# Kernel tuning notes

Measured on AMD Instinct MI355X. Metric: run time of the kernel, lower is better.

Reference implementation:

```python
import jax, jax.numpy as jnp
import numpy as np

EMB = 1024
HEADS = 16
HEAD_SZ = EMB // HEADS
EPS = 1e-5


def _layernorm(x, g, b):
    mu = jnp.mean(x, axis=-1, keepdims=True)
    var = jnp.mean(jnp.square(x - mu), axis=-1, keepdims=True)
    return (x - mu) * jax.lax.rsqrt(var + EPS) * g + b


def setup_inputs() -> dict:
    key = jax.random.key(0)
    ks = jax.random.split(key, 12)
    s_in = 1.0 / np.sqrt(EMB)
    s_h = 1.0 / np.sqrt(4 * EMB)
    return {
        "x": jax.random.normal(ks[0], (4, 1024, EMB), jnp.float32),
        # per-head Q/K/V projections stacked: [H, EMB, HEAD_SZ], no bias
        "wq": jax.random.normal(ks[1], (HEADS, EMB, HEAD_SZ), jnp.float32) * s_in,
        "wk": jax.random.normal(ks[2], (HEADS, EMB, HEAD_SZ), jnp.float32) * s_in,
        "wv": jax.random.normal(ks[3], (HEADS, EMB, HEAD_SZ), jnp.float32) * s_in,
        "w_proj": jax.random.normal(ks[4], (EMB, EMB), jnp.float32) * s_in,
        "b_proj": jnp.zeros((EMB,), jnp.float32),
        "w1": jax.random.normal(ks[5], (EMB, 4 * EMB), jnp.float32) * s_in,
        "b1": jnp.zeros((4 * EMB,), jnp.float32),
        "w2": jax.random.normal(ks[6], (4 * EMB, EMB), jnp.float32) * s_h,
        "b2": jnp.zeros((EMB,), jnp.float32),
        "g1": jnp.ones((EMB,), jnp.float32),
        "be1": jnp.zeros((EMB,), jnp.float32),
        "g2": jnp.ones((EMB,), jnp.float32),
        "be2": jnp.zeros((EMB,), jnp.float32),
    }


def reference(x, wq, wk, wv, w_proj, b_proj, w1, b1, w2, b2, g1, be1, g2, be2):
    B, T, C = x.shape
    # --- self-attention (pre-norm) ---
    h = _layernorm(x, g1, be1)
    q = jnp.einsum("btc,hcd->bhtd", h, wq)
    k = jnp.einsum("btc,hcd->bhtd", h, wk)
    v = jnp.einsum("btc,hcd->bhtd", h, wv)
    scale = 1.0 / jnp.sqrt(jnp.asarray(HEAD_SZ, x.dtype))
    scores = jnp.einsum("bhtd,bhsd->bhts", q, k) * scale  # non-causal: SDPA called with no mask
    attn = jax.nn.softmax(scores, axis=-1)
    o = jnp.einsum("bhts,bhsd->bhtd", attn, v)
    o = o.transpose(0, 2, 1, 3).reshape(B, T, C)  # concat heads (same order as torch.cat)
    sa_out = o @ w_proj + b_proj
    x = x + sa_out
    # --- feed-forward; note ln2 applied twice, faithful to source ---
    t = _layernorm(x, g2, be2)
    t = _layernorm(t, g2, be2)
    ff = jax.nn.relu(t @ w1 + b1) @ w2 + b2
    return x + ff
```

## Files before the change

kernel.cpp:

```cpp
#include <hip/hip_runtime.h>
#include <hip/hip_bf16.h>
#include <math.h>
#include <stdint.h>

typedef __bf16 bf16_t;
typedef __bf16 bf16x4 __attribute__((ext_vector_type(4)));
typedef __bf16 bf16x8 __attribute__((ext_vector_type(8)));
typedef float floatx4 __attribute__((ext_vector_type(4)));

#define BM 128
#define BK 32

__device__ __forceinline__ size_t ftaddr(int m, int k, int KT) {
    return ((size_t)(m >> 4) * KT + (k >> 5)) * 512
         + (((k >> 3) & 3) * 16 + (m & 15)) * 8 + (k & 7);
}

__device__ __forceinline__ void gload16(const void* g, void* lds) {
    __builtin_amdgcn_global_load_lds(
        (__attribute__((address_space(1))) void*)(uintptr_t)g,
        (__attribute__((address_space(3))) void*)(uintptr_t)lds,
        16, 0, 0);
}

template<int N>
__device__ __forceinline__ void waitvm_barrier() {
    if constexpr (N == 0)       asm volatile("s_waitcnt vmcnt(0)\n\ts_barrier" ::: "memory");
    else if constexpr (N == 4)  asm volatile("s_waitcnt vmcnt(4)\n\ts_barrier" ::: "memory");
    else if constexpr (N == 6)  asm volatile("s_waitcnt vmcnt(6)\n\ts_barrier" ::: "memory");
    else if constexpr (N == 8)  asm volatile("s_waitcnt vmcnt(8)\n\ts_barrier" ::: "memory");
    else if constexpr (N == 12) asm volatile("s_waitcnt vmcnt(12)\n\ts_barrier" ::: "memory");
    else if constexpr (N == 16) asm volatile("s_waitcnt vmcnt(16)\n\ts_barrier" ::: "memory");
    else static_assert(N == 0, "unsupported vmcnt");
}

__device__ __forceinline__ void waitvm_barrier_rt(int n) {
    switch (n) {
    case 12: asm volatile("s_waitcnt vmcnt(12)\n\ts_barrier" ::: "memory"); break;
    case 8:  asm volatile("s_waitcnt vmcnt(8)\n\ts_barrier"  ::: "memory"); break;
    case 6:  asm volatile("s_waitcnt vmcnt(6)\n\ts_barrier"  ::: "memory"); break;
    case 4:  asm volatile("s_waitcnt vmcnt(4)\n\ts_barrier"  ::: "memory"); break;
    default: asm volatile("s_waitcnt vmcnt(0)\n\ts_barrier"  ::: "memory"); break;
    }
}

__global__ void prep_kernel(const float* __restrict__ wq, const float* __restrict__ wk,
                            const float* __restrict__ wv, const float* __restrict__ w_proj,
                            const float* __restrict__ w1, const float* __restrict__ w2,
                            bf16_t* __restrict__ WQKVT, bf16_t* __restrict__ WPROJT,
                            bf16_t* __restrict__ W1T, bf16_t* __restrict__ W2T,
                            const float* __restrict__ x, const float* __restrict__ g1,
                            const float* __restrict__ be1, bf16_t* __restrict__ HB)
{
    __shared__ __align__(16) char psm[33024];
    const int tid = threadIdx.x;
    if (blockIdx.x < 3072) {
        float (*tile)[65] = (float(*)[65])psm;
        const int idx = blockIdx.x;
        const float* in; bf16_t* out; int R, C, rt, ct; long nrow0;
        if (idx < 768) {
            const int z = idx >> 8;
            const int hd = (idx >> 4) & 15;
            rt = idx & 15; ct = 0; R = 1024; C = 64;
            in  = (z == 0 ? wq : z == 1 ? wk : wv) + hd * 65536;
            out = WQKVT; nrow0 = z * 1024 + hd * 64;
        } else if (idx < 1024) {
            const int t = idx - 768; rt = t & 15; ct = t >> 4; R = 1024; C = 1024;
            in = w_proj; out = WPROJT; nrow0 = 0;
        } else if (idx < 2048) {
            const int t = idx - 1024; rt = t & 15; ct = t >> 4; R = 1024; C = 4096;
            in = w1; out = W1T; nrow0 = 0;
        } else {
            const int t = idx - 2048; rt = t & 63; ct = t >> 6; R = 4096; C = 1024;
            in = w2; out = W2T; nrow0 = 0;
        }
        const int r0 = rt * 64, c0 = ct * 64;
        const int tr = tid >> 4;
        const int tc = (tid & 15) * 4;
#pragma unroll
        for (int rr = 0; rr < 4; rr++) {
            const int r = tr + rr * 16;
            const float4 v = *(const float4*)&in[(long)(r0 + r) * C + c0 + tc];
            tile[r][tc + 0] = v.x; tile[r][tc + 1] = v.y;
            tile[r][tc + 2] = v.z; tile[r][tc + 3] = v.w;
        }
        __syncthreads();
        const int KT = R >> 5;
        const int w = tid >> 6, l = tid & 63;
        const int c = l >> 4, rr2 = l & 15;
#pragma unroll
        for (int it = 0; it < 2; ++it) {
            const int t8 = it * 4 + w;
            const int kt = t8 >> 2;
            const int nb = t8 & 3;
            const long n = nrow0 + c0 + nb * 16 + rr2;
            const int k = r0 + kt * 32 + c * 8;
            bf16x8 o;
#pragma unroll
            for (int e = 0; e < 8; e++)
                o[e] = (bf16_t)tile[kt * 32 + c * 8 + e][nb * 16 + rr2];
            *(bf16x8*)&out[ftaddr((int)n, k, KT)] = o;
        }
    } else {
        bf16_t (*ybuf)[1032] = (bf16_t(*)[1032])psm;
        const int wave = tid >> 6, lane = tid & 63;
        const int rb = blockIdx.x - 3072;
        float4 gvv[4], bvv[4];
#pragma unroll
        for (int j = 0; j < 4; j++) {
            gvv[j] = ((const float4*)g1)[lane + j * 64];
            bvv[j] = ((const float4*)be1)[lane + j * 64];
        }
#pragma unroll
        for (int rr = 0; rr < 4; ++rr) {
            const int lrow = wave * 4 + rr;
            const float* xr = x + (size_t)(rb * 16 + lrow) * 1024;
            float4 v[4];
            float s = 0.f, s2 = 0.f;
#pragma unroll
            for (int j = 0; j < 4; j++) {
                v[j] = ((const float4*)xr)[lane + j * 64];
                s  += v[j].x + v[j].y + v[j].z + v[j].w;
                s2 += v[j].x * v[j].x + v[j].y * v[j].y + v[j].z * v[j].z + v[j].w * v[j].w;
            }
#pragma unroll
            for (int off = 32; off >= 1; off >>= 1) {
                s  += __shfl_xor(s, off);
                s2 += __shfl_xor(s2, off);
            }
            const float mu = s * (1.0f / 1024.0f);
            const float rs = rsqrtf(fmaxf(s2 * (1.0f / 1024.0f) - mu * mu, 0.f) + 1e-5f);
#pragma unroll
            for (int j = 0; j < 4; j++) {
                bf16x4 o;
                o[0] = (bf16_t)((v[j].x - mu) * rs * gvv[j].x + bvv[j].x);
                o[1] = (bf16_t)((v[j].y - mu) * rs * gvv[j].y + bvv[j].y);
                o[2] = (bf16_t)((v[j].z - mu) * rs * gvv[j].z + bvv[j].z);
                o[3] = (bf16_t)((v[j].w - mu) * rs * gvv[j].w + bvv[j].w);
                *(bf16x4*)&ybuf[lrow][(lane + j * 64) * 4] = o;
            }
        }
        __syncthreads();
        bf16_t* outBase = HB + (size_t)rb * 32 * 512;
#pragma unroll
        for (int it = 0; it < 8; ++it) {
            const int s = it * 256 + tid;
            const int kt = s >> 6, c = (s >> 4) & 3, rr2 = s & 15;
            const bf16x8 val = *(const bf16x8*)&ybuf[rr2][kt * 32 + c * 8];
            *(bf16x8*)&outBase[(size_t)s * 8] = val;
        }
    }
}

__global__ void ln2x_kernel(const float* __restrict__ x, const float* __restrict__ g,
                            const float* __restrict__ b, bf16_t* __restrict__ outb)
{
    __shared__ __align__(16) bf16_t ybuf[16][1032];
    const int tid = threadIdx.x, wave = tid >> 6, lane = tid & 63;
    const int rb = blockIdx.x;
    float4 gvv[4], bvv[4];
#pragma unroll
    for (int j = 0; j < 4; j++) {
        gvv[j] = ((const float4*)g)[lane + j * 64];
        bvv[j] = ((const float4*)b)[lane + j * 64];
    }
#pragma unroll
    for (int rr = 0; rr < 4; ++rr) {
        const int lrow = wave * 4 + rr;
        const float* xr = x + (size_t)(rb * 16 + lrow) * 1024;
        float4 v[4];
        float s = 0.f, s2 = 0.f;
#pragma unroll
        for (int j = 0; j < 4; j++) {
            v[j] = ((const float4*)xr)[lane + j * 64];
            s  += v[j].x + v[j].y + v[j].z + v[j].w;
            s2 += v[j].x * v[j].x + v[j].y * v[j].y + v[j].z * v[j].z + v[j].w * v[j].w;
        }
#pragma unroll
        for (int off = 32; off >= 1; off >>= 1) {
            s  += __shfl_xor(s, off);
            s2 += __shfl_xor(s2, off);
        }
        float mu = s * (1.0f / 1024.0f);
        float rs = rsqrtf(fmaxf(s2 * (1.0f / 1024.0f) - mu * mu, 0.f) + 1e-5f);
        s = 0.f; s2 = 0.f;
#pragma unroll
        for (int j = 0; j < 4; j++) {
            v[j].x = (v[j].x - mu) * rs * gvv[j].x + bvv[j].x;
            v[j].y = (v[j].y - mu) * rs * gvv[j].y + bvv[j].y;
            v[j].z = (v[j].z - mu) * rs * gvv[j].z + bvv[j].z;
            v[j].w = (v[j].w - mu) * rs * gvv[j].w + bvv[j].w;
            s  += v[j].x + v[j].y + v[j].z + v[j].w;
            s2 += v[j].x * v[j].x + v[j].y * v[j].y + v[j].z * v[j].z + v[j].w * v[j].w;
        }
#pragma unroll
        for (int off = 32; off >= 1; off >>= 1) {
            s  += __shfl_xor(s, off);
            s2 += __shfl_xor(s2, off);
        }
        mu = s * (1.0f / 1024.0f);
        rs = rsqrtf(fmaxf(s2 * (1.0f / 1024.0f) - mu * mu, 0.f) + 1e-5f);
#pragma unroll
        for (int j = 0; j < 4; j++) {
            bf16x4 o;
            o[0] = (bf16_t)((v[j].x - mu) * rs * gvv[j].x + bvv[j].x);
            o[1] = (bf16_t)((v[j].y - mu) * rs * gvv[j].y + bvv[j].y);
            o[2] = (bf16_t)((v[j].z - mu) * rs * gvv[j].z + bvv[j].z);
            o[3] = (bf16_t)((v[j].w - mu) * rs * gvv[j].w + bvv[j].w);
            *(bf16x4*)&ybuf[lrow][(lane + j * 64) * 4] = o;
        }
    }
    __syncthreads();
    bf16_t* outBase = outb + (size_t)rb * 32 * 512;
#pragma unroll
    for (int it = 0; it < 8; ++it) {
        const int s = it * 256 + tid;
        const int kt = s >> 6, c = (s >> 4) & 3, rr2 = s & 15;
        const bf16x8 val = *(const bf16x8*)&ybuf[rr2][kt * 32 + c * 8];
        *(bf16x8*)&outBase[(size_t)s * 8] = val;
    }
}

template<int EPI>
__global__ __launch_bounds__(256, 2)
void gemm_ra(const bf16_t* __restrict__ A, const bf16_t* __restrict__ Bt,
             const int K, const float* __restrict__ bias,
             const float* __restrict__ resid, float* __restrict__ outf,
             const int Nout)
{
    constexpr int D = 12;
    __shared__ __align__(16) bf16_t Bs[D * 2048];
    const int tid = threadIdx.x, wave = tid >> 6, lane = tid & 63;
    const int bm = blockIdx.x * BM, bn = blockIdx.y * 64;
    const int KT = K >> 5;
    const int NT = K >> 5;
    const int NTm = NT - 1;

    floatx4 acc[2][4];
#pragma unroll
    for (int i = 0; i < 2; i++)
#pragma unroll
        for (int j = 0; j < 4; j++) acc[i][j] = (floatx4){0.f, 0.f, 0.f, 0.f};

    const bf16_t* gA0 = A + ((size_t)(bm / 16 + wave * 2 + 0) * KT) * 512 + lane * 8;
    const bf16_t* gA1 = A + ((size_t)(bm / 16 + wave * 2 + 1) * KT) * 512 + lane * 8;
    const bf16_t* gB  = Bt + ((size_t)(bn / 16 + wave) * KT) * 512 + lane * 8;

    auto stageB = [&](int t, int b) {
        gload16(gB + (size_t)t * 512, Bs + b * 2048 + wave * 512);
    };
    auto loadA = [&](bf16x8& r0, bf16x8& r1, int t) {
        const bf16_t* p0 = gA0 + (size_t)t * 512;
        const bf16_t* p1 = gA1 + (size_t)t * 512;
        asm volatile("global_load_dwordx4 %0, %1, off"
                     : "=&v"(r0) : "v"(p0) : "memory");
        asm volatile("global_load_dwordx4 %0, %1, off"
                     : "=&v"(r1) : "v"(p1) : "memory");
    };
    auto computeS = [&](const bf16x8& a0, const bf16x8& a1, int b) {
        bf16x8 bfv[4];
#pragma unroll
        for (int j = 0; j < 4; j++)
            bfv[j] = *(const bf16x8*)&Bs[b * 2048 + j * 512 + lane * 8];
#pragma unroll
        for (int j = 0; j < 4; j++) {
            acc[0][j] = __builtin_amdgcn_mfma_f32_16x16x32_bf16(a0, bfv[j], acc[0][j], 0, 0, 0);
            acc[1][j] = __builtin_amdgcn_mfma_f32_16x16x32_bf16(a1, bfv[j], acc[1][j], 0, 0, 0);
        }
    };

    bf16x8 R[4][2];
#pragma unroll
    for (int i = 0; i < 4; i++) loadA(R[i][0], R[i][1], i);
#pragma unroll
    for (int s = 0; s < 8; s++) stageB(s, s);
    asm volatile("s_waitcnt vmcnt(4)\n\ts_barrier" ::: "memory");

    int bu = 0;
    const int NTI = NT >> 2;
    for (int T = 0; T < NTI; T++) {
        const int t = T << 2;
        if (T) asm volatile("s_waitcnt vmcnt(12)\n\ts_barrier" ::: "memory");
#pragma unroll
        for (int i = 0; i < 4; i++) {
            int bs = bu + 8 + i; if (bs >= D) bs -= D;
            stageB((t + 8 + i) & NTm, bs);
            asm volatile("s_waitcnt vmcnt(10)" ::: "memory");
            __builtin_amdgcn_sched_barrier(0);
            int bc = bu + i; if (bc >= D) bc -= D;
            computeS(R[i][0], R[i][1], bc);
            loadA(R[i][0], R[i][1], (t + 4 + i) & NTm);
        }
        bu += 4; if (bu >= D) bu -= D;
    }
    asm volatile("s_waitcnt vmcnt(0)" ::: "memory");

    const int er = (lane >> 4) * 4, ec = lane & 15;
#pragma unroll
    for (int i = 0; i < 2; i++) {
#pragma unroll
        for (int j = 0; j < 4; j++) {
            const int col = bn + j * 16 + ec;
#pragma unroll
            for (int r = 0; r < 4; r++) {
                const int row = bm + wave * 32 + i * 16 + er + r;
                const size_t idx = (size_t)row * Nout + col;
                outf[idx] = acc[i][j][r] + bias[col] + resid[idx];
            }
        }
    }
}

template<int EPI, int BNt, int DEPTH>
__global__ __launch_bounds__(256, 2)
void gemm_bt(const bf16_t* __restrict__ A, const bf16_t* __restrict__ Bt,
             const int K,
             const float* __restrict__ bias, const float* __restrict__ resid,
             float* __restrict__ outf, bf16_t* __restrict__ outb,
             bf16_t* __restrict__ aux1, bf16_t* __restrict__ aux2,
             const int Nout)
{
    constexpr int NFRAG = (BNt == 256) ? 8 : 4;
    constexpr int AI    = 4;
    constexpr int LPS   = (BNt == 256) ? 6 : 4;
    constexpr int BFT   = BNt / 16;
    constexpr int ASZ = DEPTH * 8 * 512;
    constexpr int BSZ = DEPTH * BFT * 512;
    __shared__ __align__(16) bf16_t smem[ASZ + BSZ];
    bf16_t* Asb = smem;
    bf16_t* Bsb = smem + ASZ;
    const int tid  = threadIdx.x;
    const int wave = tid >> 6, lane = tid & 63;
    const int wr = wave >> 1, wc = wave & 1;
    const int bm = blockIdx.x * BM, bn = blockIdx.y * BNt;
    const int KT = K >> 5;

    floatx4 acc[AI][NFRAG];
#pragma unroll
    for (int i = 0; i < AI; i++)
#pragma unroll
        for (int j = 0; j < NFRAG; j++) acc[i][j] = (floatx4){0.f, 0.f, 0.f, 0.f};

    const bf16_t* gA0 = A + ((size_t)(bm / 16 + wave * 2 + 0) * KT) * 512 + lane * 8;
    const bf16_t* gA1 = A + ((size_t)(bm / 16 + wave * 2 + 1) * KT) * 512 + lane * 8;
    const int lA0 = (wave * 2 + 0) * 512;
    const int lA1 = (wave * 2 + 1) * 512;

    const bf16_t* gB[4];
    if (BNt == 256) {
#pragma unroll
        for (int q = 0; q < 4; q++)
            gB[q] = Bt + ((size_t)(bn / 16 + wave * 4 + q) * KT) * 512 + lane * 8;
    } else {
        gB[0] = Bt + ((size_t)(bn / 16 + wave * 2 + 0) * KT) * 512 + lane * 8;
        gB[1] = Bt + ((size_t)(bn / 16 + wave * 2 + 1) * KT) * 512 + lane * 8;
    }

    auto stage = [&](int t, int bu) {
        const size_t off = (size_t)t * 512;
        gload16(gA0 + off, Asb + bu * 4096 + lA0);
        gload16(gA1 + off, Asb + bu * 4096 + lA1);
        if (BNt == 256) {
#pragma unroll
            for (int q = 0; q < 4; q++)
                gload16(gB[q] + off, Bsb + bu * (BFT * 512) + (wave * 4 + q) * 512);
        } else {
            gload16(gB[0] + off, Bsb + bu * 4096 + lA0);
            gload16(gB[1] + off, Bsb + bu * 4096 + lA1);
        }
    };

    auto compute = [&](int bu) {
        bf16x8 af[AI], bfv[NFRAG];
#pragma unroll
        for (int i = 0; i < AI; i++)
            af[i] = *(const bf16x8*)&Asb[bu * 4096 + (wr * 4 + i) * 512 + lane * 8];
#pragma unroll
        for (int j = 0; j < NFRAG; j++)
            bfv[j] = *(const bf16x8*)&Bsb[bu * (BFT * 512) + (wc * NFRAG + j) * 512 + lane * 8];
#pragma unroll
        for (int i = 0; i < AI; i++)
#pragma unroll
            for (int j = 0; j < NFRAG; j++)
                acc[i][j] = __builtin_amdgcn_mfma_f32_16x16x32_bf16(af[i], bfv[j], acc[i][j], 0, 0, 0);
    };

    const int NT = K / BK;
#pragma unroll
    for (int i = 0; i < DEPTH - 1; ++i) stage(i, i);
    int bu = 0;
    for (int t = 0; t <= NT - DEPTH; ++t) {
        waitvm_barrier<LPS * (DEPTH - 2)>();
        stage(t + DEPTH - 1, bu == 0 ? DEPTH - 1 : bu - 1);
        compute(bu);
        bu = (bu + 1 == DEPTH) ? 0 : bu + 1;
    }
#pragma unroll
    for (int j = DEPTH - 2; j >= 0; --j) {
        waitvm_barrier_rt(LPS * j);
        compute(bu);
        bu = (bu + 1 == DEPTH) ? 0 : bu + 1;
    }

    const int er = (lane >> 4) * 4, ec = lane & 15;
    if constexpr (EPI == 0) {
        if (bn >= 2048) {
            __syncthreads();
            bf16_t* scr = smem;
#pragma unroll
            for (int i = 0; i < AI; i++)
#pragma unroll
                for (int j = 0; j < NFRAG; j++)
#pragma unroll
                    for (int r = 0; r < 4; r++)
                        scr[((wc * NFRAG + j) * 16 + ec) * 136 + (wr * 4 + i) * 16 + er + r] =
                            (bf16_t)acc[i][j][r];
            __syncthreads();
            const int bq = bm >> 10, tmod = bm & 1023, h0 = (bn - 2048) >> 6;
#pragma unroll
            for (int it = 0; it < 8; ++it) {
                const int c = it * 256 + tid;
                const int dl = c >> 4, t16 = c & 15;
                const bf16x8 val = *(const bf16x8*)&scr[dl * 136 + t16 * 8];
                const int h = h0 + (dl >> 6), dd = dl & 63;
                *(bf16x8*)&aux2[(size_t)((bq * 16 + h) * 64 + dd) * 1024 + tmod + t16 * 8] = val;
            }
            return;
        }
    }
#pragma unroll
    for (int i = 0; i < AI; i++) {
#pragma unroll
        for (int j = 0; j < NFRAG; j++) {
            const int col = bn + (wc * NFRAG + j) * 16 + ec;
#pragma unroll
            for (int r = 0; r < 4; r++) {
                const int row = bm + (wr * 4 + i) * 16 + er + r;
                const float v = acc[i][j][r];
                if (EPI == 0) {
                    const int b = row >> 10, t = row & 1023;
                    if (col < 1024) {
                        const int h = col >> 6, d = col & 63;
                        outb[(size_t)((b * 16 + h) * 1024 + t) * 64 + d] = (bf16_t)v;
                    } else {
                        const int c2 = col - 1024, h = c2 >> 6, d = c2 & 63;
                        aux1[(size_t)((b * 16 + h) * 1024 + t) * 64 + d] = (bf16_t)v;
                    }
                } else if (EPI == 2) {
                    outb[ftaddr(row, col, Nout >> 5)] = (bf16_t)fmaxf(v + bias[col], 0.f);
                }
            }
        }
    }
}

__global__ __launch_bounds__(256, 4)
void attn_kernel(const bf16_t* __restrict__ Q, const bf16_t* __restrict__ Kg,
                 const bf16_t* __restrict__ Vt, bf16_t* __restrict__ Og)
{
    __shared__ __align__(16) bf16_t Ks[2][4096];
    __shared__ __align__(16) bf16_t Vs[2][4096];
    __shared__ __align__(16) bf16_t Ps[4][1024];
    const int tid = threadIdx.x, wave = tid >> 6, lane = tid & 63;
    const int lin = blockIdx.x + (blockIdx.y << 4);
    const int xcd = lin & 7, idx = lin >> 3;
    const int bh = xcd * 8 + (idx >> 4);
    const int qt = idx & 15;
    const int b = bh >> 4, h = bh & 15;
    const int q0 = qt * 64 + wave * 16;
    const bf16_t* Qb = Q + (size_t)bh * 65536;
    const char* Kb = (const char*)(Kg + (size_t)bh * 65536);
    const char* Vb = (const char*)(Vt + (size_t)bh * 65536);
    const int fr = lane & 15, g = lane >> 4, fk = g * 8;

    const bf16x8 qf0 = *(const bf16x8*)&Qb[(size_t)(q0 + fr) * 64 + fk];
    const bf16x8 qf1 = *(const bf16x8*)&Qb[(size_t)(q0 + fr) * 64 + 32 + fk];

    floatx4 o[4];
#pragma unroll
    for (int dt = 0; dt < 4; dt++) o[dt] = (floatx4){0.f, 0.f, 0.f, 0.f};
    float lsum[4] = {0.f, 0.f, 0.f, 0.f};
    bf16_t* pw = &Ps[wave][0];
    const float sscale = 0.125f * 1.44269504088896f;

    const int sub = lane >> 3;
    const int cc  = (lane & 7) ^ sub;
    auto stage = [&](int s0, int bu) {
#pragma unroll
        for (int t = 0; t < 2; t++) {
            const int j = wave * 2 + t;
            const int row = j * 8 + sub;
            gload16(Kb + (size_t)(s0 + row) * 128 + cc * 16, &Ks[bu][j * 512]);
            gload16(Vb + (size_t)row * 2048 + (size_t)s0 * 2 + cc * 16, &Vs[bu][j * 512]);
        }
    };

    stage(0, 0);
    int bu = 0;
    for (int it = 0; it < 16; ++it) {
        __syncthreads();
        if (it < 15) stage((it + 1) * 64, bu ^ 1);
        const bf16_t* Kl = Ks[bu];
        const bf16_t* Vl = Vs[bu];

        floatx4 sacc[4];
#pragma unroll
        for (int ss = 0; ss < 4; ss++) sacc[ss] = (floatx4){0.f, 0.f, 0.f, 0.f};
        __builtin_amdgcn_s_setprio(1);
#pragma unroll
        for (int ss = 0; ss < 4; ss++) {
#pragma unroll
            for (int c = 0; c < 2; c++) {
                const int ch = c * 4 + g;
                const bf16x8 qf = (c == 0) ? qf0 : qf1;
                const bf16x8 kf = *(const bf16x8*)
                    &Kl[(ss * 16 + fr) * 64 + ((ch ^ (fr & 7)) << 3)];
                sacc[ss] = __builtin_amdgcn_mfma_f32_16x16x32_bf16(qf, kf, sacc[ss], 0, 0, 0);
            }
        }
        __builtin_amdgcn_s_setprio(0);
#pragma unroll
        for (int ss = 0; ss < 2; ss++) {
#pragma unroll
            for (int r = 0; r < 4; r++) {
                const float p = __builtin_amdgcn_exp2f(sacc[ss][r] * sscale);
                lsum[r] += p;
                const int q = g * 4 + r;
                pw[(ss * 2 + (fr >> 3)) * 128 + q * 8 + (fr & 7)] = (bf16_t)p;
            }
        }
        asm volatile("s_waitcnt lgkmcnt(0)" ::: "memory");
#pragma unroll
        for (int ss = 2; ss < 4; ss++) {
#pragma unroll
            for (int r = 0; r < 4; r++) {
                const float p = __builtin_amdgcn_exp2f(sacc[ss][r] * sscale);
                lsum[r] += p;
                const int q = g * 4 + r;
                pw[(ss * 2 + (fr >> 3)) * 128 + q * 8 + (fr & 7)] = (bf16_t)p;
            }
        }
        {
            const int ch = g;
            const bf16x8 pf = *(const bf16x8*)&pw[ch * 128 + fr * 8];
            __builtin_amdgcn_s_setprio(1);
#pragma unroll
            for (int dt = 0; dt < 4; dt++) {
                const bf16x8 vf = *(const bf16x8*)
                    &Vl[(dt * 16 + fr) * 64 + ((ch ^ (fr & 7)) << 3)];
                o[dt] = __builtin_amdgcn_mfma_f32_16x16x32_bf16(pf, vf, o[dt], 0, 0, 0);
            }
            __builtin_amdgcn_s_setprio(0);
        }
        asm volatile("s_waitcnt lgkmcnt(0)" ::: "memory");
        {
            const int ch = 4 + g;
            const bf16x8 pf = *(const bf16x8*)&pw[ch * 128 + fr * 8];
            __builtin_amdgcn_s_setprio(1);
#pragma unroll
            for (int dt = 0; dt < 4; dt++) {
                const bf16x8 vf = *(const bf16x8*)
                    &Vl[(dt * 16 + fr) * 64 + ((ch ^ (fr & 7)) << 3)];
                o[dt] = __builtin_amdgcn_mfma_f32_16x16x32_bf16(pf, vf, o[dt], 0, 0, 0);
            }
            __builtin_amdgcn_s_setprio(0);
        }
        asm volatile("" ::: "memory");
        bu ^= 1;
    }
#pragma unroll
    for (int r = 0; r < 4; r++) {
        float l = lsum[r];
        l += __shfl_xor(l, 1);
        l += __shfl_xor(l, 2);
        l += __shfl_xor(l, 4);
        l += __shfl_xor(l, 8);
        lsum[r] = 1.0f / l;
    }
    const int tq = q0 + g * 4;
#pragma unroll
    for (int dt = 0; dt < 4; dt++) {
#pragma unroll
        for (int r = 0; r < 4; r++) {
            const int m = b * 1024 + tq + r;
            const int k = h * 64 + dt * 16 + fr;
            Og[ftaddr(m, k, 32)] = (bf16_t)(o[dt][r] * lsum[r]);
        }
    }
}

extern "C" void kernel_launch(void* const* d_in, const int* in_sizes, int n_in,
                              void* d_out, int out_size, void* d_ws, size_t ws_size,
                              hipStream_t stream)
{
    const float* x      = (const float*)d_in[0];
    const float* wq     = (const float*)d_in[1];
    const float* wk     = (const float*)d_in[2];
    const float* wv     = (const float*)d_in[3];
    const float* w_proj = (const float*)d_in[4];
    const float* b_proj = (const float*)d_in[5];
    const float* w1     = (const float*)d_in[6];
    const float* b1     = (const float*)d_in[7];
    const float* w2     = (const float*)d_in[8];
    const float* b2     = (const float*)d_in[9];
    const float* g1     = (const float*)d_in[10];
    const float* be1    = (const float*)d_in[11];
    const float* g2     = (const float*)d_in[12];
    const float* be2    = (const float*)d_in[13];
    float* out = (float*)d_out;
    char* ws = (char*)d_ws;

    bf16_t* WQKVT = (bf16_t*)(ws + 0x0000000);
    bf16_t* WPROJT= (bf16_t*)(ws + 0x0600000);
    bf16_t* W1T   = (bf16_t*)(ws + 0x0800000);
    bf16_t* W2T   = (bf16_t*)(ws + 0x1000000);
    bf16_t* HB    = (bf16_t*)(ws + 0x1800000);
    bf16_t* Qb    = (bf16_t*)(ws + 0x2000000);
    bf16_t* Kb    = (bf16_t*)(ws + 0x2800000);
    bf16_t* Vtb   = (bf16_t*)(ws + 0x3000000);
    bf16_t* AO    = (bf16_t*)(ws + 0x3800000);
    float*  X2    = (float*)(ws + 0x4000000);
    bf16_t* TB    = (bf16_t*)(ws + 0x2800000);
    bf16_t* FF1B  = (bf16_t*)(ws + 0x5000000);

    dim3 blk(256);
    prep_kernel<<<3328, blk, 0, stream>>>(wq, wk, wv, w_proj, w1, w2,
                                          WQKVT, WPROJT, W1T, W2T,
                                          x, g1, be1, HB);
    gemm_bt<0, 128, 5><<<dim3(32, 24), blk, 0, stream>>>(HB, WQKVT, 1024, nullptr, nullptr,
                                                         nullptr, Qb, Kb, Vtb, 3072);
    attn_kernel<<<dim3(16, 64), blk, 0, stream>>>(Qb, Kb, Vtb, AO);
    gemm_ra<1><<<dim3(32, 16), blk, 0, stream>>>(AO, WPROJT, 1024, b_proj, x, X2, 1024);
    ln2x_kernel<<<256, blk, 0, stream>>>(X2, g2, be2, TB);
    gemm_bt<2, 256, 3><<<dim3(32, 16), blk, 0, stream>>>(TB, W1T, 1024, b1, nullptr,
                                                         nullptr, FF1B, nullptr, nullptr, 4096);
    gemm_ra<3><<<dim3(32, 16), blk, 0, stream>>>(FF1B, W2T, 4096, b2, X2, out, 1024);
}
```

Baseline: 287.0 us.

## Deepen A register prefetch in gemm_ra and route FFN1 through it with ReLU epilogue

Rewrites the gemm_ra main loop so A fragments are prefetched eight K-tiles ahead in registers instead of four, with one barrier per half-iteration and B staging interleaved with the A loads. Adds an EPI==2 epilogue that applies bias and ReLU and writes bf16 in the fragment-tiled layout. The FFN1 GEMM now uses this kernel with 128x64 tiles instead of gemm_bt with 256-wide tiles. The intent is better latency hiding, at the cost of more registers for the A fragments and narrower N tiles for FFN1, which lowers B reuse and launches four times as many blocks.

```diff
diff --git a/kernel.cpp b/kernel.cpp
--- a/kernel.cpp
+++ b/kernel.cpp
@@ -226,7 +226,7 @@
 void gemm_ra(const bf16_t* __restrict__ A, const bf16_t* __restrict__ Bt,
              const int K, const float* __restrict__ bias,
              const float* __restrict__ resid, float* __restrict__ outf,
-             const int Nout)
+             bf16_t* __restrict__ outb, const int Nout)
 {
     constexpr int D = 12;
     __shared__ __align__(16) bf16_t Bs[D * 2048];
@@ -269,29 +269,37 @@
         }
     };
 
-    bf16x8 R[4][2];
-#pragma unroll
-    for (int i = 0; i < 4; i++) loadA(R[i][0], R[i][1], i);
-#pragma unroll
-    for (int s = 0; s < 8; s++) stageB(s, s);
-    asm volatile("s_waitcnt vmcnt(4)\n\ts_barrier" ::: "memory");
+    bf16x8 R[8][2];
+#pragma unroll
+    for (int i = 0; i < 4; i++) {
+        stageB(i, i);
+        loadA(R[i][0], R[i][1], i);
+    }
+#pragma unroll
+    for (int i = 0; i < 4; i++) {
+        stageB(4 + i, 4 + i);
+        loadA(R[4 + i][0], R[4 + i][1], 4 + i);
+    }
 
     int bu = 0;
-    const int NTI = NT >> 2;
-    for (int T = 0; T < NTI; T++) {
-        const int t = T << 2;
-        if (T) asm volatile("s_waitcnt vmcnt(12)\n\ts_barrier" ::: "memory");
-#pragma unroll
-        for (int i = 0; i < 4; i++) {
-            int bs = bu + 8 + i; if (bs >= D) bs -= D;
-            stageB((t + 8 + i) & NTm, bs);
-            asm volatile("s_waitcnt vmcnt(10)" ::: "memory");
+    const int NU = NT >> 3;
+    for (int U = 0; U < NU; U++) {
+        const int t = U << 3;
+#pragma unroll
+        for (int hf = 0; hf < 2; hf++) {
+            const int th = t + hf * 4;
+            asm volatile("s_waitcnt vmcnt(12)\n\ts_barrier" ::: "memory");
             __builtin_amdgcn_sched_barrier(0);
-            int bc = bu + i; if (bc >= D) bc -= D;
-            computeS(R[i][0], R[i][1], bc);
-            loadA(R[i][0], R[i][1], (t + 4 + i) & NTm);
-        }
-        bu += 4; if (bu >= D) bu -= D;
+#pragma unroll
+            for (int i = 0; i < 4; i++) {
+                int bs = bu + 8 + i; if (bs >= D) bs -= D;
+                stageB((th + 8 + i) & NTm, bs);
+                int bc = bu + i; if (bc >= D) bc -= D;
+                computeS(R[hf * 4 + i][0], R[hf * 4 + i][1], bc);
+                loadA(R[hf * 4 + i][0], R[hf * 4 + i][1], (th + 8 + i) & NTm);
+            }
+            bu += 4; if (bu >= D) bu -= D;
+        }
     }
     asm volatile("s_waitcnt vmcnt(0)" ::: "memory");
 
@@ -304,8 +312,13 @@
 #pragma unroll
             for (int r = 0; r < 4; r++) {
                 const int row = bm + wave * 32 + i * 16 + er + r;
-                const size_t idx = (size_t)row * Nout + col;
-                outf[idx] = acc[i][j][r] + bias[col] + resid[idx];
+                const float v = acc[i][j][r];
+                if (EPI == 2) {
+                    outb[ftaddr(row, col, Nout >> 5)] = (bf16_t)fmaxf(v + bias[col], 0.f);
+                } else {
+                    const size_t idx = (size_t)row * Nout + col;
+                    outf[idx] = v + bias[col] + resid[idx];
+                }
             }
         }
     }
@@ -630,9 +643,11 @@
     gemm_bt<0, 128, 5><<<dim3(32, 24), blk, 0, stream>>>(HB, WQKVT, 1024, nullptr, nullptr,
                                                          nullptr, Qb, Kb, Vtb, 3072);
     attn_kernel<<<dim3(16, 64), blk, 0, stream>>>(Qb, Kb, Vtb, AO);
-    gemm_ra<1><<<dim3(32, 16), blk, 0, stream>>>(AO, WPROJT, 1024, b_proj, x, X2, 1024);
+    gemm_ra<1><<<dim3(32, 16), blk, 0, stream>>>(AO, WPROJT, 1024, b_proj, x, X2,
+                                                 nullptr, 1024);
     ln2x_kernel<<<256, blk, 0, stream>>>(X2, g2, be2, TB);
-    gemm_bt<2, 256, 3><<<dim3(32, 16), blk, 0, stream>>>(TB, W1T, 1024, b1, nullptr,
-                                                         nullptr, FF1B, nullptr, nullptr, 4096);
-    gemm_ra<3><<<dim3(32, 16), blk, 0, stream>>>(FF1B, W2T, 4096, b2, X2, out, 1024);
-}
+    gemm_ra<2><<<dim3(32, 64), blk, 0, stream>>>(TB, W1T, 1024, b1, nullptr, nullptr,
+                                                 FF1B, 4096);
+    gemm_ra<3><<<dim3(32, 16), blk, 0, stream>>>(FF1B, W2T, 4096, b2, X2, out,
+                                                 nullptr, 1024);
+}
```

Measured after the change: 303.0 us. +5.6%, slower.
